# Optimization experiments

Hardware: AMD Instinct MI355X
Metric: run time of the kernel (lower is better)

The kernel has to match this reference:

```python
import jax, jax.numpy as jnp
from jax import lax
import numpy as np

THRESH = 0.5   # LIF firing threshold (STBP defaults)
LENS = 0.5     # surrogate-gradient window half-width
DECAY = 0.2    # membrane decay
EPS = 1e-5

N_NODES = 20000
C_IN = 128
C_OUT = 64
T = 8
E = 160000


@jax.custom_vjp
def spike_fn(u):
    return (u > THRESH).astype(u.dtype)

def _spike_fwd(u):
    return spike_fn(u), u

def _spike_bwd(u, g):
    # rectangular surrogate: grad passes where |u - thresh| < lens
    return (g * (jnp.abs(u - THRESH) < LENS).astype(g.dtype),)

spike_fn.defvjp(_spike_fwd, _spike_bwd)


def setup_inputs() -> dict:
    key = jax.random.key(0)
    k1, k2, k3, k4, k5 = jax.random.split(key, 5)
    x = jax.random.normal(k1, (N_NODES, C_IN, T), dtype=jnp.float32)
    edge_index = jax.random.randint(k2, (2, E), 0, N_NODES, dtype=jnp.int64)
    gamma = jnp.ones((C_IN,), dtype=jnp.float32)
    beta = jnp.zeros((C_IN,), dtype=jnp.float32)
    s0 = 1.0 / np.sqrt(C_IN)
    W0 = jax.random.uniform(k3, (C_OUT, C_IN), jnp.float32, -s0, s0)  # k=0 hop weights
    W1 = jax.random.uniform(k4, (C_OUT, C_IN), jnp.float32, -s0, s0)  # k=1 hop weights
    b = jax.random.uniform(k5, (C_OUT,), jnp.float32, -s0, s0)
    return {"x": x, "edge_index": edge_index, "gamma": gamma, "beta": beta,
            "W0": W0, "W1": W1, "b": b}


def _ebnorm(x, gamma, beta):
    # BatchNorm1d over [N, C, T]: stats per channel across nodes and time
    mean = jnp.mean(x, axis=(0, 2), keepdims=True)
    var = jnp.mean((x - mean) ** 2, axis=(0, 2), keepdims=True)
    return gamma[None, :, None] * (x - mean) * lax.rsqrt(var + EPS) + beta[None, :, None]


def _lif(x):
    # x: [N, C, T]; iterate membrane over time with reset-by-subtraction-free STBP dynamics
    xt = jnp.moveaxis(x, -1, 0)  # [T, N, C]
    zeros = jnp.zeros_like(xt[0])

    def step(carry, inp):
        mem, sp = carry
        mem = mem * DECAY * (1.0 - sp) + inp
        sp = spike_fn(mem)
        return (mem, sp), sp

    _, spikes = lax.scan(step, (zeros, zeros), xt)
    return jnp.moveaxis(spikes, 0, -1)  # [N, C, T]


def _tagconv(x, edge_index, W0, W1, b):
    # TAGConv K=1 with GCN normalization (no self loops), applied per time step
    src, dst = edge_index[0], edge_index[1]
    n = x.shape[0]
    deg = jax.ops.segment_sum(jnp.ones_like(dst, dtype=x.dtype), dst, num_segments=n)
    dinv = jnp.where(deg > 0, lax.rsqrt(jnp.maximum(deg, 1e-12)), 0.0)
    w = dinv[src] * dinv[dst]                       # [E]
    msg = x[src] * w[:, None, None]                 # [E, C, T]
    agg = jax.ops.segment_sum(msg, dst, num_segments=n)  # [N, C, T]
    out = jnp.einsum('nct,dc->ndt', x, W0) + jnp.einsum('nct,dc->ndt', agg, W1)
    return out + b[None, :, None]


def reference(x, edge_index, gamma, beta, W0, W1, b):
    h = _ebnorm(x, gamma, beta)
    s = _lif(h)
    return _tagconv(s, edge_index, W0, W1, b)
```

## Files before the change

kernel.cpp:

```cpp
#include <hip/hip_runtime.h>
#include <stdint.h>
#include <math.h>

#define N_NODES 20000
#define C_IN 128
#define C_OUT 64
#define T_STEPS 8
#define NE 160000
#define NB_STATS 1024
#define NPB 8
#define RPAD 264

typedef __attribute__((ext_vector_type(8))) short short8;
typedef __attribute__((ext_vector_type(4))) float f32x4;

static __device__ __forceinline__ unsigned short bf16_rne(float f) {
  unsigned u = __builtin_bit_cast(unsigned, f);
  return (unsigned short)((u + 0x7FFFu + ((u >> 16) & 1u)) >> 16);
}

__global__ __launch_bounds__(256) void stats_kernel(const float* __restrict__ x,
                                                    double* __restrict__ dsum,
                                                    double* __restrict__ dsq) {
  const int P = N_NODES * C_IN;
  int tid = threadIdx.x;
  int gid = blockIdx.x * 256 + tid;
  double s = 0.0, q = 0.0;
  for (int p = gid; p < P; p += 256 * NB_STATS) {
    const float4* xp = (const float4*)(x + (size_t)p * 8);
    float4 a = xp[0], b = xp[1];
    float v[8] = {a.x, a.y, a.z, a.w, b.x, b.y, b.z, b.w};
#pragma unroll
    for (int j = 0; j < 8; ++j) { double d = (double)v[j]; s += d; q += d * d; }
  }
  __shared__ double ls[256], lq[256];
  ls[tid] = s; lq[tid] = q;
  __syncthreads();
  if (tid < 128) {
    dsum[tid * NB_STATS + blockIdx.x] = ls[tid] + ls[tid + 128];
    dsq [tid * NB_STATS + blockIdx.x] = lq[tid] + lq[tid + 128];
  }
}

__global__ __launch_bounds__(256) void finalize_kernel(const double* __restrict__ dsum,
                                                       const double* __restrict__ dsq,
                                                       const float* __restrict__ gamma,
                                                       const float* __restrict__ beta,
                                                       double* __restrict__ adbl,
                                                       double* __restrict__ bdbl) {
  int c = blockIdx.x, tid = threadIdx.x;
  __shared__ double ls[256], lq[256];
  double s = 0.0, q = 0.0;
#pragma unroll
  for (int i = 0; i < NB_STATS / 256; ++i) {
    s += dsum[c * NB_STATS + tid + 256 * i];
    q += dsq [c * NB_STATS + tid + 256 * i];
  }
  ls[tid] = s; lq[tid] = q;
  __syncthreads();
  for (int o = 128; o > 0; o >>= 1) {
    if (tid < o) { ls[tid] += ls[tid + o]; lq[tid] += lq[tid + o]; }
    __syncthreads();
  }
  if (tid == 0) {
    const double cnt = (double)N_NODES * T_STEPS;
    double mean = ls[0] / cnt;
    double var  = lq[0] / cnt - mean * mean;
    double ai = (double)gamma[c] / sqrt(var + 1e-5);
    adbl[c] = ai;
    bdbl[c] = (double)beta[c] - mean * ai;
  }
}

__global__ __launch_bounds__(256) void lif_kernel(const float* __restrict__ x,
                                                  const double* __restrict__ adbl,
                                                  const double* __restrict__ bdbl,
                                                  unsigned char* __restrict__ spk) {
  int p = blockIdx.x * 256 + threadIdx.x;
  int c = p & (C_IN - 1);
  const float4* xp = (const float4*)(x + (size_t)p * 8);
  float4 a4 = xp[0], b4 = xp[1];
  float v[8] = {a4.x, a4.y, a4.z, a4.w, b4.x, b4.y, b4.z, b4.w};
  double a = adbl[c], bb = bdbl[c];
  double mem = 0.0, sp = 0.0;
  unsigned byte = 0;
#pragma unroll
  for (int t = 0; t < 8; ++t) {
    double h = a * (double)v[t] + bb;
    mem = mem * (0.2 * (1.0 - sp)) + h;
    int fire = mem > 0.5;
    sp = fire ? 1.0 : 0.0;
    byte |= (unsigned)fire << t;
  }
  spk[p] = (unsigned char)byte;
}

__global__ __launch_bounds__(256) void deg_kernel(const int* __restrict__ ei, int* __restrict__ deg) {
  int e = blockIdx.x * 256 + threadIdx.x;
  if (e < NE) atomicAdd(&deg[ei[NE + e]], 1);
}

__global__ __launch_bounds__(1024) void scan_kernel(const int* __restrict__ deg,
                                                    int* __restrict__ offs,
                                                    int* __restrict__ cursor,
                                                    float* __restrict__ dinv) {
  __shared__ int wsum[16];
  int tid = threadIdx.x, lane = tid & 63, w = tid >> 6;
  int carry = 0;
  for (int base = 0; base < N_NODES; base += 1024) {
    int i = base + tid;
    int v = (i < N_NODES) ? deg[i] : 0;
    int s = v;
#pragma unroll
    for (int o = 1; o < 64; o <<= 1) {
      int u = __shfl_up(s, o);
      if (lane >= o) s += u;
    }
    if (lane == 63) wsum[w] = s;
    __syncthreads();
    int wpre = 0;
    for (int j = 0; j < w; ++j) wpre += wsum[j];
    int excl = carry + wpre + (s - v);
    if (i < N_NODES) {
      offs[i] = excl; cursor[i] = excl;
      dinv[i] = v > 0 ? (float)(1.0 / sqrt((double)v)) : 0.f;
    }
    int tot = 0;
#pragma unroll
    for (int j = 0; j < 16; ++j) tot += wsum[j];
    carry += tot;
    __syncthreads();
  }
  if (tid == 0) offs[N_NODES] = carry;
}

__global__ __launch_bounds__(256) void fill_kernel(const int* __restrict__ ei,
                                                   int* __restrict__ cursor,
                                                   int* __restrict__ csr) {
  int e = blockIdx.x * 256 + threadIdx.x;
  if (e < NE) {
    int pos = atomicAdd(&cursor[ei[NE + e]], 1);
    csr[pos] = ei[e];
  }
}

__global__ __launch_bounds__(256) void wtb_kernel(const float* __restrict__ W0,
                                                  const float* __restrict__ W1,
                                                  unsigned short* __restrict__ WTb) {
  int idx = blockIdx.x * 256 + threadIdx.x;
  int mt = idx >> 9, kt = (idx >> 6) & 7, lane = idx & 63;
  int m = mt * 16 + (lane & 15);
  int kb = kt * 32 + (lane >> 4) * 8;
  unsigned short frag[8];
#pragma unroll
  for (int j = 0; j < 8; ++j) {
    int k = kb + j;
    float wv = (k < 128) ? W0[m * 128 + k] : W1[m * 128 + (k - 128)];
    frag[j] = bf16_rne(wv);
  }
  *(uint4*)&WTb[(size_t)idx * 8] = *(uint4*)frag;
}

__global__ __launch_bounds__(256) void main_kernel(const unsigned char* __restrict__ spk,
                                                   const int* __restrict__ offs,
                                                   const int* __restrict__ csr,
                                                   const float* __restrict__ dinv,
                                                   const unsigned short* __restrict__ WTb,
                                                   const float* __restrict__ bias,
                                                   float* __restrict__ out) {
  __shared__ unsigned short Bls[64 * RPAD];
  int tid = threadIdx.x;
  int n0 = blockIdx.x * NPB;
  int lane = tid & 63, w = tid >> 6;

#pragma unroll
  for (int it = 0; it < 2; ++it) {
    int task = tid + it * 256;
    int col = task & 63, cg = task >> 6;
    int node = n0 + (col >> 3), t = col & 7;
    uint4 u = *(const uint4*)(spk + (size_t)node * 128 + cg * 16);
    unsigned ua[4] = {u.x, u.y, u.z, u.w};
    unsigned ow[8];
#pragma unroll
    for (int i = 0; i < 4; ++i) {
      unsigned v = (ua[i] >> t) & 0x01010101u;
      unsigned s0 = (v & 1u)         ? 0x3F80u : 0u;
      unsigned s1 = ((v >> 8) & 1u)  ? 0x3F800000u : 0u;
      unsigned s2 = ((v >> 16) & 1u) ? 0x3F80u : 0u;
      unsigned s3 = (v >> 24)        ? 0x3F800000u : 0u;
      ow[i * 2]     = s0 | s1;
      ow[i * 2 + 1] = s2 | s3;
    }
    uint4 o0 = {ow[0], ow[1], ow[2], ow[3]};
    uint4 o1 = {ow[4], ow[5], ow[6], ow[7]};
    *(uint4*)&Bls[col * RPAD + cg * 16]     = o0;
    *(uint4*)&Bls[col * RPAD + cg * 16 + 8] = o1;
  }

  const unsigned short* sp16 = (const unsigned short*)spk;
#pragma unroll 1
  for (int nn = 0; nn < 2; ++nn) {
    int node = n0 + w * 2 + nn;
    int e0 = offs[node], e1 = offs[node + 1];
    float acc[16];
#pragma unroll
    for (int j = 0; j < 16; ++j) acc[j] = 0.f;
    for (int e = e0; e < e1; ++e) {
      int src = csr[e];
      float wt = dinv[src];
      unsigned bits = sp16[(size_t)src * 64 + lane];
#pragma unroll
      for (int j = 0; j < 16; ++j)
        acc[j] = fmaf((float)((bits >> j) & 1u), wt, acc[j]);
    }
    float sc = dinv[node];
    int colb = (w * 2 + nn) * 8;
    int c0 = 2 * lane;
#pragma unroll
    for (int t = 0; t < 8; ++t) {
      unsigned pk = (unsigned)bf16_rne(acc[t] * sc) |
                    ((unsigned)bf16_rne(acc[8 + t] * sc) << 16);
      *(unsigned*)&Bls[(colb + t) * RPAD + 128 + c0] = pk;
    }
  }
  __syncthreads();

  int q = lane >> 4, l16 = lane & 15;
  int col = w * 16 + l16;
  const short8* WT8 = (const short8*)WTb;
  f32x4 acc0 = {0, 0, 0, 0}, acc1 = {0, 0, 0, 0}, acc2 = {0, 0, 0, 0}, acc3 = {0, 0, 0, 0};
#pragma unroll
  for (int kt = 0; kt < 8; ++kt) {
    short8 b = *(const short8*)&Bls[col * RPAD + kt * 32 + q * 8];
    acc0 = __builtin_amdgcn_mfma_f32_16x16x32_bf16(WT8[(0 * 8 + kt) * 64 + lane], b, acc0, 0, 0, 0);
    acc1 = __builtin_amdgcn_mfma_f32_16x16x32_bf16(WT8[(1 * 8 + kt) * 64 + lane], b, acc1, 0, 0, 0);
    acc2 = __builtin_amdgcn_mfma_f32_16x16x32_bf16(WT8[(2 * 8 + kt) * 64 + lane], b, acc2, 0, 0, 0);
    acc3 = __builtin_amdgcn_mfma_f32_16x16x32_bf16(WT8[(3 * 8 + kt) * 64 + lane], b, acc3, 0, 0, 0);
  }

  int node = n0 + (col >> 3), t = col & 7;
  float* ob = out + (size_t)node * 512 + t;
  f32x4 av[4] = {acc0, acc1, acc2, acc3};
#pragma unroll
  for (int mt = 0; mt < 4; ++mt) {
#pragma unroll
    for (int r = 0; r < 4; ++r) {
      int d = mt * 16 + q * 4 + r;
      ob[d * 8] = av[mt][r] + bias[d];
    }
  }
}

extern "C" void kernel_launch(void* const* d_in, const int* in_sizes, int n_in,
                              void* d_out, int out_size, void* d_ws, size_t ws_size,
                              hipStream_t stream) {
  const float* x     = (const float*)d_in[0];
  const int*   ei    = (const int*)d_in[1];
  const float* gamma = (const float*)d_in[2];
  const float* beta  = (const float*)d_in[3];
  const float* W0    = (const float*)d_in[4];
  const float* W1    = (const float*)d_in[5];
  const float* bias  = (const float*)d_in[6];
  float* out = (float*)d_out;

  char* ws = (char*)d_ws;
  size_t off = 0;
  auto alloc = [&](size_t bytes) -> void* {
    void* p = ws + off;
    off = (off + bytes + 255) & ~(size_t)255;
    return p;
  };
  double* dsum = (double*)alloc(128 * NB_STATS * 8);
  double* dsq  = (double*)alloc(128 * NB_STATS * 8);
  double* adbl = (double*)alloc(128 * 8);
  double* bdbl = (double*)alloc(128 * 8);
  int*    deg  = (int*)alloc(N_NODES * 4);
  float*  dinv = (float*)alloc(N_NODES * 4);
  int*    offs = (int*)alloc((N_NODES + 1) * 4);
  int*    curs = (int*)alloc(N_NODES * 4);
  int*    csr  = (int*)alloc(NE * 4);
  unsigned char* spk = (unsigned char*)alloc((size_t)N_NODES * C_IN);
  unsigned short* WTb = (unsigned short*)alloc(2048 * 8 * 2);

  hipMemsetAsync(deg, 0, N_NODES * 4, stream);

  stats_kernel<<<NB_STATS, 256, 0, stream>>>(x, dsum, dsq);
  finalize_kernel<<<128, 256, 0, stream>>>(dsum, dsq, gamma, beta, adbl, bdbl);
  lif_kernel<<<(N_NODES * C_IN) / 256, 256, 0, stream>>>(x, adbl, bdbl, spk);
  deg_kernel<<<(NE + 255) / 256, 256, 0, stream>>>(ei, deg);
  scan_kernel<<<1, 1024, 0, stream>>>(deg, offs, curs, dinv);
  fill_kernel<<<(NE + 255) / 256, 256, 0, stream>>>(ei, curs, csr);
  wtb_kernel<<<8, 256, 0, stream>>>(W0, W1, WTb);
  main_kernel<<<N_NODES / NPB, 256, 0, stream>>>(spk, offs, csr, dinv, WTb, bias, out);
}
```

Before: 261.1 us.

## Merge small kernels, single-pass scan, and widen main kernel to 512 threads

Folds the degree count into the stats kernel and the weight conversion into the finalize kernel as extra blocks, which removes two launches. The scan becomes a single pass in which each thread handles 20 nodes, replacing 20 block-serial iterations. The main kernel now runs 512 threads with one node per wave, unrolls the gather loop by four to get more loads in flight, and splits the MFMA work so each wave computes one output row tile for two column tiles. These changes cut launch overhead and serial latency, at the cost of higher register pressure and more branching inside the fused kernels.

```diff
diff --git a/kernel.cpp b/kernel.cpp
--- a/kernel.cpp
+++ b/kernel.cpp
@@ -8,6 +8,7 @@
 #define T_STEPS 8
 #define NE 160000
 #define NB_STATS 1024
+#define NB_DEG ((NE + 255) / 256)
 #define NPB 8
 #define RPAD 264
 
@@ -19,11 +20,18 @@
   return (unsigned short)((u + 0x7FFFu + ((u >> 16) & 1u)) >> 16);
 }
 
-__global__ __launch_bounds__(256) void stats_kernel(const float* __restrict__ x,
-                                                    double* __restrict__ dsum,
-                                                    double* __restrict__ dsq) {
+__global__ __launch_bounds__(256) void stats_deg_kernel(const float* __restrict__ x,
+                                                        double* __restrict__ dsum,
+                                                        double* __restrict__ dsq,
+                                                        const int* __restrict__ ei,
+                                                        int* __restrict__ deg) {
+  int tid = threadIdx.x;
+  if (blockIdx.x >= NB_STATS) {
+    int e = (blockIdx.x - NB_STATS) * 256 + tid;
+    if (e < NE) atomicAdd(&deg[ei[NE + e]], 1);
+    return;
+  }
   const int P = N_NODES * C_IN;
-  int tid = threadIdx.x;
   int gid = blockIdx.x * 256 + tid;
   double s = 0.0, q = 0.0;
   for (int p = gid; p < P; p += 256 * NB_STATS) {
@@ -42,13 +50,32 @@
   }
 }
 
-__global__ __launch_bounds__(256) void finalize_kernel(const double* __restrict__ dsum,
-                                                       const double* __restrict__ dsq,
-                                                       const float* __restrict__ gamma,
-                                                       const float* __restrict__ beta,
-                                                       double* __restrict__ adbl,
-                                                       double* __restrict__ bdbl) {
-  int c = blockIdx.x, tid = threadIdx.x;
+__global__ __launch_bounds__(256) void finalize_wtb_kernel(const double* __restrict__ dsum,
+                                                           const double* __restrict__ dsq,
+                                                           const float* __restrict__ gamma,
+                                                           const float* __restrict__ beta,
+                                                           double* __restrict__ adbl,
+                                                           double* __restrict__ bdbl,
+                                                           const float* __restrict__ W0,
+                                                           const float* __restrict__ W1,
+                                                           unsigned short* __restrict__ WTb) {
+  int tid = threadIdx.x;
+  if (blockIdx.x >= 128) {
+    int idx = (blockIdx.x - 128) * 256 + tid;
+    int mt = idx >> 9, kt = (idx >> 6) & 7, lane = idx & 63;
+    int m = mt * 16 + (lane & 15);
+    int kb = kt * 32 + (lane >> 4) * 8;
+    unsigned short frag[8];
+#pragma unroll
+    for (int j = 0; j < 8; ++j) {
+      int k = kb + j;
+      float wv = (k < 128) ? W0[m * 128 + k] : W1[m * 128 + (k - 128)];
+      frag[j] = bf16_rne(wv);
+    }
+    *(uint4*)&WTb[(size_t)idx * 8] = *(uint4*)frag;
+    return;
+  }
+  int c = blockIdx.x;
   __shared__ double ls[256], lq[256];
   double s = 0.0, q = 0.0;
 #pragma unroll
@@ -95,43 +122,42 @@
   spk[p] = (unsigned char)byte;
 }
 
-__global__ __launch_bounds__(256) void deg_kernel(const int* __restrict__ ei, int* __restrict__ deg) {
-  int e = blockIdx.x * 256 + threadIdx.x;
-  if (e < NE) atomicAdd(&deg[ei[NE + e]], 1);
-}
-
 __global__ __launch_bounds__(1024) void scan_kernel(const int* __restrict__ deg,
                                                     int* __restrict__ offs,
                                                     int* __restrict__ cursor,
                                                     float* __restrict__ dinv) {
+  int tid = threadIdx.x, lane = tid & 63, w = tid >> 6;
+  int base = tid * 20;
+  int v[20];
+  int s = 0;
+#pragma unroll
+  for (int i = 0; i < 20; ++i) {
+    int n = base + i;
+    int d = (n < N_NODES) ? deg[n] : 0;
+    v[i] = d; s += d;
+  }
+  int p = s;
+#pragma unroll
+  for (int o = 1; o < 64; o <<= 1) {
+    int u = __shfl_up(p, o);
+    if (lane >= o) p += u;
+  }
   __shared__ int wsum[16];
-  int tid = threadIdx.x, lane = tid & 63, w = tid >> 6;
-  int carry = 0;
-  for (int base = 0; base < N_NODES; base += 1024) {
-    int i = base + tid;
-    int v = (i < N_NODES) ? deg[i] : 0;
-    int s = v;
-#pragma unroll
-    for (int o = 1; o < 64; o <<= 1) {
-      int u = __shfl_up(s, o);
-      if (lane >= o) s += u;
-    }
-    if (lane == 63) wsum[w] = s;
-    __syncthreads();
-    int wpre = 0;
-    for (int j = 0; j < w; ++j) wpre += wsum[j];
-    int excl = carry + wpre + (s - v);
-    if (i < N_NODES) {
-      offs[i] = excl; cursor[i] = excl;
-      dinv[i] = v > 0 ? (float)(1.0 / sqrt((double)v)) : 0.f;
-    }
-    int tot = 0;
-#pragma unroll
-    for (int j = 0; j < 16; ++j) tot += wsum[j];
-    carry += tot;
-    __syncthreads();
-  }
-  if (tid == 0) offs[N_NODES] = carry;
+  if (lane == 63) wsum[w] = p;
+  __syncthreads();
+  int wpre = 0;
+  for (int j = 0; j < w; ++j) wpre += wsum[j];
+  int excl = wpre + p - s;
+#pragma unroll
+  for (int i = 0; i < 20; ++i) {
+    int n = base + i;
+    if (n < N_NODES) {
+      offs[n] = excl; cursor[n] = excl;
+      dinv[n] = v[i] > 0 ? (float)(1.0 / sqrt((double)v[i])) : 0.f;
+      excl += v[i];
+    }
+  }
+  if (tid == 1023) offs[N_NODES] = excl;
 }
 
 __global__ __launch_bounds__(256) void fill_kernel(const int* __restrict__ ei,
@@ -144,24 +170,7 @@
   }
 }
 
-__global__ __launch_bounds__(256) void wtb_kernel(const float* __restrict__ W0,
-                                                  const float* __restrict__ W1,
-                                                  unsigned short* __restrict__ WTb) {
-  int idx = blockIdx.x * 256 + threadIdx.x;
-  int mt = idx >> 9, kt = (idx >> 6) & 7, lane = idx & 63;
-  int m = mt * 16 + (lane & 15);
-  int kb = kt * 32 + (lane >> 4) * 8;
-  unsigned short frag[8];
-#pragma unroll
-  for (int j = 0; j < 8; ++j) {
-    int k = kb + j;
-    float wv = (k < 128) ? W0[m * 128 + k] : W1[m * 128 + (k - 128)];
-    frag[j] = bf16_rne(wv);
-  }
-  *(uint4*)&WTb[(size_t)idx * 8] = *(uint4*)frag;
-}
-
-__global__ __launch_bounds__(256) void main_kernel(const unsigned char* __restrict__ spk,
+__global__ __launch_bounds__(512) void main_kernel(const unsigned char* __restrict__ spk,
                                                    const int* __restrict__ offs,
                                                    const int* __restrict__ csr,
                                                    const float* __restrict__ dinv,
@@ -173,21 +182,19 @@
   int n0 = blockIdx.x * NPB;
   int lane = tid & 63, w = tid >> 6;
 
-#pragma unroll
-  for (int it = 0; it < 2; ++it) {
-    int task = tid + it * 256;
-    int col = task & 63, cg = task >> 6;
+  {
+    int col = tid & 63, cg = tid >> 6;
     int node = n0 + (col >> 3), t = col & 7;
     uint4 u = *(const uint4*)(spk + (size_t)node * 128 + cg * 16);
     unsigned ua[4] = {u.x, u.y, u.z, u.w};
     unsigned ow[8];
 #pragma unroll
     for (int i = 0; i < 4; ++i) {
-      unsigned v = (ua[i] >> t) & 0x01010101u;
-      unsigned s0 = (v & 1u)         ? 0x3F80u : 0u;
-      unsigned s1 = ((v >> 8) & 1u)  ? 0x3F800000u : 0u;
-      unsigned s2 = ((v >> 16) & 1u) ? 0x3F80u : 0u;
-      unsigned s3 = (v >> 24)        ? 0x3F800000u : 0u;
+      unsigned vv = (ua[i] >> t) & 0x01010101u;
+      unsigned s0 = (vv & 1u)         ? 0x3F80u : 0u;
+      unsigned s1 = ((vv >> 8) & 1u)  ? 0x3F800000u : 0u;
+      unsigned s2 = ((vv >> 16) & 1u) ? 0x3F80u : 0u;
+      unsigned s3 = (vv >> 24)        ? 0x3F800000u : 0u;
       ow[i * 2]     = s0 | s1;
       ow[i * 2 + 1] = s2 | s3;
     }
@@ -197,15 +204,32 @@
     *(uint4*)&Bls[col * RPAD + cg * 16 + 8] = o1;
   }
 
-  const unsigned short* sp16 = (const unsigned short*)spk;
+  {
+    int node = n0 + w;
+    int e0 = offs[node], e1 = offs[node + 1];
+    const unsigned short* sp16 = (const unsigned short*)spk;
+    float acc[16];
+#pragma unroll
+    for (int j = 0; j < 16; ++j) acc[j] = 0.f;
+    int e = e0;
 #pragma unroll 1
-  for (int nn = 0; nn < 2; ++nn) {
-    int node = n0 + w * 2 + nn;
-    int e0 = offs[node], e1 = offs[node + 1];
-    float acc[16];
-#pragma unroll
-    for (int j = 0; j < 16; ++j) acc[j] = 0.f;
-    for (int e = e0; e < e1; ++e) {
+    for (; e + 4 <= e1; e += 4) {
+      int s0 = csr[e], s1 = csr[e + 1], s2 = csr[e + 2], s3 = csr[e + 3];
+      float w0 = dinv[s0], w1 = dinv[s1], w2 = dinv[s2], w3 = dinv[s3];
+      unsigned b0 = sp16[(size_t)s0 * 64 + lane];
+      unsigned b1 = sp16[(size_t)s1 * 64 + lane];
+      unsigned b2 = sp16[(size_t)s2 * 64 + lane];
+      unsigned b3 = sp16[(size_t)s3 * 64 + lane];
+#pragma unroll
+      for (int j = 0; j < 16; ++j) {
+        acc[j] = fmaf((float)((b0 >> j) & 1u), w0, acc[j]);
+        acc[j] = fmaf((float)((b1 >> j) & 1u), w1, acc[j]);
+        acc[j] = fmaf((float)((b2 >> j) & 1u), w2, acc[j]);
+        acc[j] = fmaf((float)((b3 >> j) & 1u), w3, acc[j]);
+      }
+    }
+#pragma unroll 1
+    for (; e < e1; ++e) {
       int src = csr[e];
       float wt = dinv[src];
       unsigned bits = sp16[(size_t)src * 64 + lane];
@@ -214,7 +238,7 @@
         acc[j] = fmaf((float)((bits >> j) & 1u), wt, acc[j]);
     }
     float sc = dinv[node];
-    int colb = (w * 2 + nn) * 8;
+    int colb = w * 8;
     int c0 = 2 * lane;
 #pragma unroll
     for (int t = 0; t < 8; ++t) {
@@ -226,28 +250,29 @@
   __syncthreads();
 
   int q = lane >> 4, l16 = lane & 15;
-  int col = w * 16 + l16;
+  int mt = w & 3, ct0 = w >> 2, ct1 = ct0 + 2;
+  int colA = ct0 * 16 + l16, colB = ct1 * 16 + l16;
   const short8* WT8 = (const short8*)WTb;
-  f32x4 acc0 = {0, 0, 0, 0}, acc1 = {0, 0, 0, 0}, acc2 = {0, 0, 0, 0}, acc3 = {0, 0, 0, 0};
+  f32x4 acc0 = {0, 0, 0, 0}, acc1 = {0, 0, 0, 0};
 #pragma unroll
   for (int kt = 0; kt < 8; ++kt) {
-    short8 b = *(const short8*)&Bls[col * RPAD + kt * 32 + q * 8];
-    acc0 = __builtin_amdgcn_mfma_f32_16x16x32_bf16(WT8[(0 * 8 + kt) * 64 + lane], b, acc0, 0, 0, 0);
-    acc1 = __builtin_amdgcn_mfma_f32_16x16x32_bf16(WT8[(1 * 8 + kt) * 64 + lane], b, acc1, 0, 0, 0);
-    acc2 = __builtin_amdgcn_mfma_f32_16x16x32_bf16(WT8[(2 * 8 + kt) * 64 + lane], b, acc2, 0, 0, 0);
-    acc3 = __builtin_amdgcn_mfma_f32_16x16x32_bf16(WT8[(3 * 8 + kt) * 64 + lane], b, acc3, 0, 0, 0);
-  }
-
-  int node = n0 + (col >> 3), t = col & 7;
-  float* ob = out + (size_t)node * 512 + t;
-  f32x4 av[4] = {acc0, acc1, acc2, acc3};
-#pragma unroll
-  for (int mt = 0; mt < 4; ++mt) {
-#pragma unroll
-    for (int r = 0; r < 4; ++r) {
-      int d = mt * 16 + q * 4 + r;
-      ob[d * 8] = av[mt][r] + bias[d];
-    }
+    short8 a = WT8[(mt * 8 + kt) * 64 + lane];
+    short8 bA = *(const short8*)&Bls[colA * RPAD + kt * 32 + q * 8];
+    short8 bB = *(const short8*)&Bls[colB * RPAD + kt * 32 + q * 8];
+    acc0 = __builtin_amdgcn_mfma_f32_16x16x32_bf16(a, bA, acc0, 0, 0, 0);
+    acc1 = __builtin_amdgcn_mfma_f32_16x16x32_bf16(a, bB, acc1, 0, 0, 0);
+  }
+
+  int nodeA = n0 + (colA >> 3), tA = colA & 7;
+  int nodeB = n0 + (colB >> 3), tB = colB & 7;
+  float* obA = out + (size_t)nodeA * 512 + tA;
+  float* obB = out + (size_t)nodeB * 512 + tB;
+#pragma unroll
+  for (int r = 0; r < 4; ++r) {
+    int d = mt * 16 + q * 4 + r;
+    float bv = bias[d];
+    obA[d * 8] = acc0[r] + bv;
+    obB[d * 8] = acc1[r] + bv;
   }
 }
 
@@ -284,12 +309,10 @@
 
   hipMemsetAsync(deg, 0, N_NODES * 4, stream);
 
-  stats_kernel<<<NB_STATS, 256, 0, stream>>>(x, dsum, dsq);
-  finalize_kernel<<<128, 256, 0, stream>>>(dsum, dsq, gamma, beta, adbl, bdbl);
+  stats_deg_kernel<<<NB_STATS + NB_DEG, 256, 0, stream>>>(x, dsum, dsq, ei, deg);
+  finalize_wtb_kernel<<<128 + 8, 256, 0, stream>>>(dsum, dsq, gamma, beta, adbl, bdbl, W0, W1, WTb);
   lif_kernel<<<(N_NODES * C_IN) / 256, 256, 0, stream>>>(x, adbl, bdbl, spk);
-  deg_kernel<<<(NE + 255) / 256, 256, 0, stream>>>(ei, deg);
   scan_kernel<<<1, 1024, 0, stream>>>(deg, offs, curs, dinv);
   fill_kernel<<<(NE + 255) / 256, 256, 0, stream>>>(ei, curs, csr);
-  wtb_kernel<<<8, 256, 0, stream>>>(W0, W1, WTb);
-  main_kernel<<<N_NODES / NPB, 256, 0, stream>>>(spk, offs, csr, dinv, WTb, bias, out);
-}
+  main_kernel<<<N_NODES / NPB, 512, 0, stream>>>(spk, offs, csr, dinv, WTb, bias, out);
+}
```

Result: faster. 235.8 us (-9.7%).
